# Kernel optimization log

Hardware: AMD Instinct MI355X
Metric: run time of the kernel (lower is better)

The kernel has to match this reference:

```python
import jax, jax.numpy as jnp
import numpy as np

# static config (matches init_kwargs / source constants)
B, S, CCH, NF, T = 64, 50, 3, 129, 29   # batch, seq, channels, freq bins (nfft/2+1), frames
M_FB = 32                                # filterbank size M in F1
D = 16                                   # latents -> SPD matrix size
M_OFF = D * (D - 1) // 2                 # strictly-lower Cholesky entries
HID = D + M_OFF                          # ODE state size
ODE_U = 256                              # n_units
NCLS = 5
K_EULER, DT = 4, 0.25                    # fixed-step Euler ODE solve per interval
BN_EPS = 1e-5


def lin_tri_filter(nfilt=M_FB, nfft=256, samplerate=100):
    # faithful port of FilterbankShape.lin_tri_filter_shape
    highfreq = samplerate / 2
    hz = np.linspace(0, highfreq, nfilt + 2)
    b = np.floor((nfft + 1) * hz / samplerate)
    fb = np.zeros([nfilt, nfft // 2 + 1])
    for j in range(nfilt):
        for i in range(int(b[j]), int(b[j + 1])):
            fb[j, i] = (i - b[j]) / (b[j + 1] - b[j])
        for i in range(int(b[j + 1]), int(b[j + 2])):
            fb[j, i] = (b[j + 2] - i) / (b[j + 2] - b[j + 1])
    return fb.T.astype(np.float32)  # (129, 32)


def setup_inputs() -> dict:
    key = jax.random.key(0)
    ks = jax.random.split(key, 32)
    f32 = jnp.float32
    CIN = CCH * M_FB  # 96

    def unif(k, shape, bound):
        return jax.random.uniform(k, shape, f32, -bound, bound)

    sd = 1.0 / np.sqrt(D)
    so = 1.0 / np.sqrt(M_OFF)
    cb1 = 1.0 / np.sqrt(CIN * 5)
    cb2 = 1.0 / np.sqrt(CIN * 5)
    lb = lambda fan_in: 1.0 / np.sqrt(fan_in)

    inp = {
        "x": jax.random.normal(ks[0], (B, S, CCH, NF, T), f32),
        "fw": jax.nn.sigmoid(jax.random.normal(ks[1], (NF, M_FB), f32)),
        "s_tri": jnp.asarray(lin_tri_filter()),
        "conv1_w": unif(ks[2], (CIN, CIN, 5), cb1),
        "conv1_b": unif(ks[3], (CIN,), cb1),
        "bn1_g": jnp.ones((CIN,), f32),
        "bn1_b": jnp.zeros((CIN,), f32),
        "conv2_w": unif(ks[4], (D, CIN, 5), cb2),
        "conv2_b": unif(ks[5], (D,), cb2),
        "bn2_g": jnp.ones((D,), f32),
        "bn2_b": jnp.zeros((D,), f32),
        "wx_d": unif(ks[6], (D, 3 * D), sd),
        "wh_d": unif(ks[7], (D, 3 * D), sd),
        "bias_d": unif(ks[8], (3 * D,), sd),
        "wx_o": unif(ks[9], (M_OFF, 3 * M_OFF), so),
        "wh_o": unif(ks[10], (M_OFF, 3 * M_OFF), so),
        "bias_o": unif(ks[11], (3 * M_OFF,), so),
        "ode_w0": unif(ks[12], (HID, ODE_U), lb(HID)),
        "ode_b0": unif(ks[13], (ODE_U,), lb(HID)),
        "ode_w1": unif(ks[14], (ODE_U, ODE_U), lb(ODE_U)),
        "ode_b1": unif(ks[15], (ODE_U,), lb(ODE_U)),
        "ode_w2": unif(ks[16], (ODE_U, ODE_U), lb(ODE_U)),
        "ode_b2": unif(ks[17], (ODE_U,), lb(ODE_U)),
        "ode_w3": unif(ks[18], (ODE_U, HID), lb(ODE_U)),
        "ode_b3": unif(ks[19], (HID,), lb(ODE_U)),
        "cls_w": unif(ks[20], (HID, NCLS), lb(HID)),
        "cls_b": unif(ks[21], (NCLS,), lb(HID)),
    }
    return inp


def _forward(x, fw, s_tri, conv1_w, conv1_b, bn1_g, bn1_b, conv2_w, conv2_b,
             bn2_g, bn2_b, wx_d, wh_d, bias_d, wx_o, wh_o, bias_o,
             ode_w0, ode_b0, ode_w1, ode_b1, ode_w2, ode_b2, ode_w3, ode_b3,
             cls_w, cls_b):
    b, s = x.shape[:2]
    # --- filter_bank: (b,s,C,F,T) x (F,M) -> (b,s,C*M,T) ---
    xf = jnp.einsum('bscft,fm->bscmt', x, fw * s_tri)
    h = xf.reshape(b * s, CCH * M_FB, T)
    dn = ('NCH', 'OIH', 'NCH')

    def conv_bn_lrelu(h, w, bias, g, be):
        h = jax.lax.conv_general_dilated(h, w, (1,), 'VALID', dimension_numbers=dn)
        h = h + bias[None, :, None]
        mu = h.mean((0, 2), keepdims=True)           # BatchNorm1d (train-mode stats)
        var = h.var((0, 2), keepdims=True)
        h = (h - mu) / jnp.sqrt(var + BN_EPS) * g[None, :, None] + be[None, :, None]
        return jnp.where(h >= 0, h, 0.01 * h)        # LeakyReLU

    h = conv_bn_lrelu(h, conv1_w, conv1_b, bn1_g, bn1_b)   # (bs, 96, 25)
    h = conv_bn_lrelu(h, conv2_w, conv2_b, bn2_g, bn2_b)   # (bs, D, 21)
    feats = h.transpose(0, 2, 1)                           # (bs, t, D)

    def oas(X):  # OAS-shrunk covariance, X: (n, d)
        n, d = X.shape
        xm = X - X.mean(0)
        emp = xm.T @ xm / (n - 1)
        mu = jnp.trace(emp) / d
        alpha = jnp.mean(emp ** 2)
        num = alpha + mu ** 2
        den = (n + 1.0) * (alpha - mu ** 2 / d)
        shr = jnp.where(den == 0, 1.0, jnp.minimum(num / den, 1.0))
        return (1.0 - shr) * emp + shr * mu * jnp.eye(d, dtype=X.dtype)

    covs = jax.vmap(oas)(feats)                            # (bs, D, D)
    L = jnp.linalg.cholesky(covs).reshape(b, s, D, D)
    ir, ic = np.tril_indices(D, -1)
    x_d = jnp.diagonal(L, axis1=-2, axis2=-1)              # (b,s,D) positive
    x_o = L[..., ir, ic]                                   # (b,s,M_OFF)

    def ode_net(hh):  # odefunc: Lin, [Tanh,Lin]*2, Tanh, Lin
        hh = hh @ ode_w0 + ode_b0
        hh = jnp.tanh(hh) @ ode_w1 + ode_b1
        hh = jnp.tanh(hh) @ ode_w2 + ode_b2
        return jnp.tanh(hh) @ ode_w3 + ode_b3

    abs_bd = jnp.abs(bias_d)

    def step(carry, xt):
        hd, ho = carry
        xd, xo = xt
        # ODE evolution of hidden state in Cholesky chart (log-diag || off-diag)
        hc = jnp.concatenate([jnp.log(hd), ho], -1)
        for _ in range(K_EULER):
            hc = hc + DT * ode_net(hc)
        hd = jnp.exp(hc[:, :D])
        ho = hc[:, D:]
        # diag RGRU cell (PosLinear + softplus; log/exp products simplify)
        gx = xd @ jnp.abs(wx_d)
        gh = hd @ jnp.abs(wh_d)
        ixr, ixi, ixn = jnp.split(gx, 3, 1)
        hhr, hhi, hhn = jnp.split(gh, 3, 1)
        br, bi, bn = jnp.split(abs_bd, 3)
        r = jax.nn.sigmoid(br * ixr * hhr)
        z = jax.nn.sigmoid(bi * ixi * hhi)
        ng = jax.nn.softplus(bn * ixn * r * hhn)
        hd = hd ** z * ng ** (1.0 - z)   # geodesic GRU update on positive diag
        # off-diag RGRU cell (standard Euclidean GRU)
        gx = xo @ wx_o
        gh = ho @ wh_o
        ixr, ixi, ixn = jnp.split(gx, 3, 1)
        hhr, hhi, hhn = jnp.split(gh, 3, 1)
        br2, bi2, bn2 = jnp.split(bias_o, 3)
        r = jax.nn.sigmoid(ixr + hhr + br2)
        z = jax.nn.sigmoid(ixi + hhi + bi2)
        ng = jnp.tanh(ixn + r * hhn + bn2)
        ho = ng + z * (ho - ng)
        return (hd, ho), None

    hd0 = jnp.ones((b, D), x.dtype)
    ho0 = jnp.zeros((b, M_OFF), x.dtype)
    (hd, ho), _ = jax.lax.scan(step, (hd0, ho0),
                               (x_d.transpose(1, 0, 2), x_o.transpose(1, 0, 2)))
    feat = jnp.concatenate([jnp.log(hd), ho], -1)
    return feat @ cls_w + cls_b  # (b, NCLS)


def reference(x, fw, s_tri, conv1_w, conv1_b, bn1_g, bn1_b, conv2_w, conv2_b,
              bn2_g, bn2_b, wx_d, wh_d, bias_d, wx_o, wh_o, bias_o,
              ode_w0, ode_b0, ode_w1, ode_b1, ode_w2, ode_b2, ode_w3, ode_b3,
              cls_w, cls_b):
    return _forward(x, fw, s_tri, conv1_w, conv1_b, bn1_g, bn1_b, conv2_w,
                    conv2_b, bn2_g, bn2_b, wx_d, wh_d, bias_d, wx_o, wh_o,
                    bias_o, ode_w0, ode_b0, ode_w1, ode_b1, ode_w2, ode_b2,
                    ode_w3, ode_b3, cls_w, cls_b)
```

## Files before the change

kernel.cpp:

```cpp
#include <hip/hip_runtime.h>
#include <math.h>


#define BB 64
#define NIMG 3200

typedef _Float16 f16;
typedef _Float16 f16x8 __attribute__((ext_vector_type(8)));
typedef float f32x4 __attribute__((ext_vector_type(4)));

#define HS 164
#define GS 516

__device__ __forceinline__ float sigm(float x) { return 1.f / (1.f + expf(-x)); }
__device__ __forceinline__ float fsigm(float x) {
  return __fdividef(1.f, 1.f + __expf(-x));
}
__device__ __forceinline__ float ftanh(float x) {
  return 1.f - __fdividef(2.f, __expf(2.f * x) + 1.f);
}

#define OFF_W0  0
#define OFF_W1  20480
#define OFF_W2  53248
#define OFF_W3  86016
#define OFF_GRZ 104448
#define OFF_GNX 135168
#define OFF_GNH 143360
#define PK2_TOT 151552

__global__ __launch_bounds__(256) void k1_fb(const float* __restrict__ x,
                                             const float* __restrict__ fw,
                                             const float* __restrict__ st,
                                             float* __restrict__ h1) {
  __shared__ __align__(16) float ws[129 * 32];
  __shared__ __align__(16) float xs[129 * 32];
  const int tid = threadIdx.x;
  const int n = blockIdx.x;
  const float* xp = x + (size_t)n * 11223;

  for (int i = tid; i < 4128; i += 256) ws[i] = fw[i] * st[i];

  float acc[4][4];
#pragma unroll
  for (int i = 0; i < 4; ++i)
#pragma unroll
    for (int j = 0; j < 4; ++j) acc[i][j] = 0.f;

  const int c = tid / 64;
  const int rem = tid % 64;
  const int m0 = (rem / 8) * 4;
  const int t0 = (rem % 8) * 4;

  for (int fc = 0; fc < 3; ++fc) {
    __syncthreads();
    for (int i = tid; i < 3741; i += 256) {
      int cc = i / 1247;
      int r = i - cc * 1247;
      int f = r / 29;
      int t = r - f * 29;
      xs[(cc * 43 + f) * 32 + t] = xp[cc * 3741 + (fc * 43 + f) * 29 + t];
    }
    for (int i = tid; i < 129; i += 256) {
      xs[i * 32 + 29] = 0.f; xs[i * 32 + 30] = 0.f; xs[i * 32 + 31] = 0.f;
    }
    __syncthreads();
    if (tid < 192) {
      const float* xb = xs + (c * 43) * 32 + t0;
      const float* wb = ws + (fc * 43) * 32 + m0;
      for (int f = 0; f < 43; ++f) {
        float4 xv = *(const float4*)(xb + f * 32);
        float4 wv = *(const float4*)(wb + f * 32);
        float xa[4] = {xv.x, xv.y, xv.z, xv.w};
        float wa[4] = {wv.x, wv.y, wv.z, wv.w};
#pragma unroll
        for (int i = 0; i < 4; ++i)
#pragma unroll
          for (int j = 0; j < 4; ++j) acc[i][j] += wa[i] * xa[j];
      }
    }
  }
  if (tid < 192) {
    const int nt = (t0 == 28) ? 1 : 4;
    for (int i = 0; i < 4; ++i)
      for (int j = 0; j < nt; ++j)
        h1[(size_t)n * 2784 + (size_t)(c * 32 + m0 + i) * 29 + (t0 + j)] = acc[i][j];
  }
}

__global__ __launch_bounds__(256) void k2_conv1(const float* __restrict__ h1,
                                                const float* __restrict__ w,
                                                const float* __restrict__ bias,
                                                float* __restrict__ h2,
                                                float* __restrict__ part1) {
  __shared__ __align__(16) float ins[2 * 96 * 32];
  __shared__ __align__(16) float wls[96 * 81];
  const int tid = threadIdx.x;
  const int wg = blockIdx.x;

  for (int i = tid; i < 2 * 2784; i += 256) {
    int img = i / 2784;
    int e = i - img * 2784;
    int ci = e / 29;
    int t = e - ci * 29;
    ins[img * 3072 + ci * 32 + t] = h1[(size_t)(wg * 2 + img) * 2784 + e];
  }

  const int img = tid / 96;
  const int co = tid - img * 96;
  float acc[25];
#pragma unroll
  for (int t = 0; t < 25; ++t) acc[t] = 0.f;

  for (int cc = 0; cc < 6; ++cc) {
    __syncthreads();
    for (int i = tid; i < 7680; i += 256) {
      int cw = i / 80;
      int r = i - cw * 80;
      wls[cw * 81 + r] = w[cw * 480 + cc * 80 + r];
    }
    __syncthreads();
    if (tid < 192) {
      for (int ci = 0; ci < 16; ++ci) {
        float xv[29];
#pragma unroll
        for (int j = 0; j < 29; ++j) xv[j] = ins[img * 3072 + (cc * 16 + ci) * 32 + j];
        float wv[5];
#pragma unroll
        for (int d = 0; d < 5; ++d) wv[d] = wls[co * 81 + ci * 5 + d];
#pragma unroll
        for (int t = 0; t < 25; ++t) {
          float s = acc[t];
#pragma unroll
          for (int d = 0; d < 5; ++d) s += xv[t + d] * wv[d];
          acc[t] = s;
        }
      }
    }
  }
  if (tid < 192) {
    const int n = wg * 2 + img;
    const float bval = bias[co];
    float s1 = 0.f, s2 = 0.f;
    for (int t = 0; t < 25; ++t) {
      float v = acc[t] + bval;
      h2[(size_t)n * 2400 + co * 25 + t] = v;
      s1 += v;
      s2 += v * v;
    }
    part1[((size_t)n * 96 + co) * 2 + 0] = s1;
    part1[((size_t)n * 96 + co) * 2 + 1] = s2;
  }
}

__global__ __launch_bounds__(256) void k3_bn1(const float* __restrict__ part,
                                              const float* __restrict__ gg,
                                              const float* __restrict__ be,
                                              float* __restrict__ ab) {
  __shared__ double sd[256], sq[256];
  const int c = blockIdx.x;
  const int t = threadIdx.x;
  double s = 0.0, q = 0.0;
  for (int n = t; n < NIMG; n += 256) {
    s += (double)part[((size_t)n * 96 + c) * 2 + 0];
    q += (double)part[((size_t)n * 96 + c) * 2 + 1];
  }
  sd[t] = s; sq[t] = q;
  __syncthreads();
  for (int off = 128; off > 0; off >>= 1) {
    if (t < off) { sd[t] += sd[t + off]; sq[t] += sq[t + off]; }
    __syncthreads();
  }
  if (t == 0) {
    double mu = sd[0] / 80000.0;
    double var = sq[0] / 80000.0 - mu * mu;
    float A = (float)((double)gg[c] / sqrt(var + 1e-5));
    ab[c * 2 + 0] = A;
    ab[c * 2 + 1] = (float)((double)be[c] - mu * (double)A);
  }
}

__global__ __launch_bounds__(256) void k5_bn2(const float* __restrict__ part,
                                              const float* __restrict__ gg,
                                              const float* __restrict__ be,
                                              float* __restrict__ ab) {
  __shared__ double sd[256], sq[256];
  const int c = blockIdx.x;
  const int t = threadIdx.x;
  double s = 0.0, q = 0.0;
  for (int n = t; n < 800; n += 256) {
    s += (double)part[((size_t)n * 16 + c) * 2 + 0];
    q += (double)part[((size_t)n * 16 + c) * 2 + 1];
  }
  sd[t] = s; sq[t] = q;
  __syncthreads();
  for (int off = 128; off > 0; off >>= 1) {
    if (t < off) { sd[t] += sd[t + off]; sq[t] += sq[t + off]; }
    __syncthreads();
  }
  if (t == 0) {
    double mu = sd[0] / 67200.0;
    double var = sq[0] / 67200.0 - mu * mu;
    float A = (float)((double)gg[c] / sqrt(var + 1e-5));
    ab[c * 2 + 0] = A;
    ab[c * 2 + 1] = (float)((double)be[c] - mu * (double)A);
  }
}

__global__ __launch_bounds__(256) void k4_conv2(const float* __restrict__ h2,
                                                const float* __restrict__ w,
                                                const float* __restrict__ bias,
                                                const float* __restrict__ bn1,
                                                float* __restrict__ h3,
                                                float* __restrict__ part2) {
  __shared__ __align__(16) float ins[4 * 96 * 26];
  __shared__ __align__(16) float wls[16 * 241];
  __shared__ float A1s[96], B1s[96];
  __shared__ float red[16 * 16 * 2];
  const int tid = threadIdx.x;
  const int wg = blockIdx.x;

  if (tid < 96) {
    A1s[tid] = bn1[tid * 2 + 0];
    B1s[tid] = bn1[tid * 2 + 1];
  }
  __syncthreads();
  for (int i = tid; i < 9600; i += 256) {
    int img = i / 2400;
    int e = i - img * 2400;
    int ci = e / 25;
    int t = e - ci * 25;
    float v = h2[(size_t)(wg * 4 + img) * 2400 + e];
    v = A1s[ci] * v + B1s[ci];
    v = (v >= 0.f) ? v : 0.01f * v;
    ins[img * 2496 + ci * 26 + t] = v;
  }
  for (int i = tid; i < 4 * 96; i += 256) ins[(i / 96) * 2496 + (i % 96) * 26 + 25] = 0.f;

  const int img = tid >> 6;
  const int co = (tid >> 2) & 15;
  const int tg = tid & 3;
  const int t0s[4] = {0, 6, 11, 16};
  const int t0 = t0s[tg];
  const int tl = (tg == 0) ? 6 : 5;
  float acc[6] = {0.f, 0.f, 0.f, 0.f, 0.f, 0.f};

  for (int cc = 0; cc < 2; ++cc) {
    __syncthreads();
    for (int i = tid; i < 3840; i += 256) {
      int cw = i / 240;
      int r = i - cw * 240;
      wls[cw * 241 + r] = w[cw * 480 + cc * 240 + r];
    }
    __syncthreads();
    for (int ci = 0; ci < 48; ++ci) {
      float xv[10];
#pragma unroll
      for (int j = 0; j < 10; ++j) xv[j] = ins[img * 2496 + (cc * 48 + ci) * 26 + t0 + j];
      float wv[5];
#pragma unroll
      for (int d = 0; d < 5; ++d) wv[d] = wls[co * 241 + ci * 5 + d];
#pragma unroll
      for (int t = 0; t < 6; ++t) {
        float s = acc[t];
#pragma unroll
        for (int d = 0; d < 5; ++d) s += xv[t + d] * wv[d];
        acc[t] = s;
      }
    }
  }
  const float bval = bias[co];
  float s1 = 0.f, s2 = 0.f;
  const int n = wg * 4 + img;
  for (int t = 0; t < 6; ++t) {
    if (t < tl) {
      float v = acc[t] + bval;
      h3[(size_t)n * 336 + co * 21 + t0 + t] = v;
      s1 += v;
      s2 += v * v;
    }
  }
  red[(co * 16 + img * 4 + tg) * 2 + 0] = s1;
  red[(co * 16 + img * 4 + tg) * 2 + 1] = s2;
  __syncthreads();
  if (tid < 16) {
    float s = 0.f, q = 0.f;
    for (int k = 0; k < 16; ++k) {
      s += red[(tid * 16 + k) * 2 + 0];
      q += red[(tid * 16 + k) * 2 + 1];
    }
    part2[((size_t)wg * 16 + tid) * 2 + 0] = s;
    part2[((size_t)wg * 16 + tid) * 2 + 1] = q;
  }
}

__global__ __launch_bounds__(256) void k6_oas(const float* __restrict__ h3,
                                              const float* __restrict__ bn2,
                                              float* __restrict__ xd,
                                              float* __restrict__ xo) {
  __shared__ float X[4][21 * 17 + 3];
  __shared__ float A[4][16 * 17];
  __shared__ float mcol[4][16];
  const int tid = threadIdx.x;
  const int wid = tid >> 6;
  const int lane = tid & 63;
  const int n = blockIdx.x * 4 + wid;
  const float* hp = h3 + (size_t)n * 336;

  for (int e = lane; e < 336; e += 64) {
    int c = e / 21;
    int t = e - c * 21;
    float v = hp[e];
    v = bn2[c * 2 + 0] * v + bn2[c * 2 + 1];
    v = (v >= 0.f) ? v : 0.01f * v;
    X[wid][t * 17 + c] = v;
  }
  __syncthreads();
  if (lane < 16) {
    float s = 0.f;
    for (int t = 0; t < 21; ++t) s += X[wid][t * 17 + lane];
    mcol[wid][lane] = s * (1.f / 21.f);
  }
  __syncthreads();
  for (int e = lane; e < 336; e += 64) {
    int t = e / 16;
    int c = e - t * 16;
    X[wid][t * 17 + c] -= mcol[wid][c];
  }
  __syncthreads();

  float tr_p = 0.f, al_p = 0.f;
  float ent[3];
  int ei[3], ej[3], ne = 0;
  for (int e = lane; e < 136; e += 64) {
    int i = 0, e2 = e;
    while (e2 >= 16 - i) { e2 -= 16 - i; i++; }
    int j = i + e2;
    float s = 0.f;
    for (int t = 0; t < 21; ++t) s += X[wid][t * 17 + i] * X[wid][t * 17 + j];
    s *= (1.f / 20.f);
    ent[ne] = s; ei[ne] = i; ej[ne] = j; ne++;
    if (i == j) tr_p += s;
    al_p += s * s * ((i == j) ? 1.f : 2.f);
  }
  for (int m = 1; m < 64; m <<= 1) {
    tr_p += __shfl_xor(tr_p, m);
    al_p += __shfl_xor(al_p, m);
  }
  const float mu = tr_p * (1.f / 16.f);
  const float alpha = al_p * (1.f / 256.f);
  const float num = alpha + mu * mu;
  const float den = 22.f * (alpha - mu * mu * (1.f / 16.f));
  const float shr = (den == 0.f) ? 1.f : fminf(num / den, 1.f);
  for (int q = 0; q < ne; ++q) {
    float c = (1.f - shr) * ent[q] + ((ei[q] == ej[q]) ? shr * mu : 0.f);
    A[wid][ei[q] * 17 + ej[q]] = c;
    A[wid][ej[q] * 17 + ei[q]] = c;
  }
  __syncthreads();

  for (int k = 0; k < 16; ++k) {
    float akk = A[wid][k * 17 + k];
    __syncthreads();
    float d = sqrtf(akk);
    float rd = 1.f / d;
    if (lane == k) A[wid][k * 17 + k] = d;
    if (lane > k && lane < 16) A[wid][lane * 17 + k] *= rd;
    __syncthreads();
    if (lane > k && lane < 16) {
      float Lik = A[wid][lane * 17 + k];
      for (int j = k + 1; j <= lane; ++j) A[wid][lane * 17 + j] -= Lik * A[wid][j * 17 + k];
    }
    __syncthreads();
  }
  if (lane < 16) xd[(size_t)n * 16 + lane] = A[wid][lane * 17 + lane];
  for (int p = lane; p < 120; p += 64) {
    int i = 1, p2 = p;
    while (p2 >= i) { p2 -= i; i++; }
    xo[(size_t)n * 120 + p] = A[wid][i * 17 + p2];
  }
}

__global__ __launch_bounds__(256) void k0_pack(const float* __restrict__ w0,
                                               const float* __restrict__ w1,
                                               const float* __restrict__ w2,
                                               const float* __restrict__ w3,
                                               const float* __restrict__ wxo,
                                               const float* __restrict__ who,
                                               uint32_t* __restrict__ dst) {
  int i = blockIdx.x * 256 + threadIdx.x;
  if (i >= PK2_TOT) return;
  int j = i, kind, NT;
  if (j < OFF_W1)       { kind = 0; NT = 16; }
  else if (j < OFF_W2)  { kind = 1; NT = 16; j -= OFF_W1; }
  else if (j < OFF_W3)  { kind = 2; NT = 16; j -= OFF_W2; }
  else if (j < OFF_GRZ) { kind = 3; NT = 9;  j -= OFF_W3; }
  else if (j < OFF_GNX) { kind = 4; NT = 15; j -= OFF_GRZ; }
  else if (j < OFF_GNH) { kind = 5; NT = 8;  j -= OFF_GNX; }
  else                  { kind = 6; NT = 8;  j -= OFF_GNH; }
  const int tile = j >> 8;
  const int rem = j & 255;
  const int l = rem >> 2;
  const int wd = rem & 3;
  const int t = tile / NT;
  const int nt = tile - t * NT;
  const int col = nt * 16 + (l & 15);
  const int kk = t * 32 + 8 * (l >> 4) + 2 * wd;

  float v[2];
#pragma unroll
  for (int q = 0; q < 2; ++q) {
    const int k = kk + q;
    float s = 0.f;
    if (kind == 0)      { if (k < 136) s = w0[k * 256 + col]; }
    else if (kind == 1) { s = w1[k * 256 + col]; }
    else if (kind == 2) { s = w2[k * 256 + col]; }
    else if (kind == 3) { if (col < 136) s = w3[k * 136 + col]; }
    else if (kind == 4) {
      if (k < 120) s = wxo[k * 360 + col];
      else if (k >= 128 && k < 248) s = who[(k - 128) * 360 + col];
    } else if (kind == 5) { if (k < 120 && col < 120) s = wxo[k * 360 + 240 + col]; }
    else                  { if (k < 120 && col < 120) s = who[k * 360 + 240 + col]; }
    v[q] = s;
  }
  union { f16 h[2]; uint32_t u; } cv;
  cv.h[0] = (f16)v[0];
  cv.h[1] = (f16)v[1];
  dst[i] = cv.u;
}

__device__ __forceinline__ uint4 aread_lin(const f16* X, int t, int l) {
  return ((const uint4*)X)[t * 64 + l];
}
__device__ __forceinline__ void xwrite_frag(f16* X, int row, int col, float v) {
  const int slot = row + 16 * ((col >> 3) & 3);
  const int byte = (((col >> 5) * 64 + slot) << 4) + 2 * (col & 7);
  *(f16*)((char*)X + byte) = (f16)v;
}

union UF { uint4 u; f16x8 h; };

template <int KT, int NT, int MODE>
__device__ __forceinline__ void mlp_one(const f16* __restrict__ Xin,
                                        const uint4* __restrict__ B,
                                        const float* __restrict__ bias,
                                        f16* __restrict__ Xout,
                                        float* __restrict__ hcf,
                                        f16* __restrict__ Xnext,
                                        float* __restrict__ ehl,
                                        int nt, int l) {
  if (nt < 0 || nt >= NT) return;
  const int m = l & 15;
  const int g = l >> 4;
  uint4 bf[KT];
#pragma unroll
  for (int t = 0; t < KT; ++t) bf[t] = B[(t * NT + nt) * 64 + l];
  uint4 af[KT];
#pragma unroll
  for (int t = 0; t < KT; ++t) af[t] = aread_lin(Xin, t, l);
  f32x4 acc = {0.f, 0.f, 0.f, 0.f};
#pragma unroll
  for (int t = 0; t < KT; ++t) {
    UF a; a.u = af[t];
    UF b; b.u = bf[t];
    acc = __builtin_amdgcn_mfma_f32_16x16x32_f16(a.h, b.h, acc, 0, 0, 0);
  }
  const int col = nt * 16 + m;
  if (MODE == 0) {
    const float bb = bias[col];
#pragma unroll
    for (int i2 = 0; i2 < 4; ++i2)
      xwrite_frag(Xout, 4 * g + i2, col, ftanh(acc[i2] + bb));
  } else {
    if (col < 136) {
      const float bb = bias[col];
#pragma unroll
      for (int i2 = 0; i2 < 4; ++i2) {
        const int row = 4 * g + i2;
        float v = hcf[row * HS + col] + 0.25f * (acc[i2] + bb);
        hcf[row * HS + col] = v;
        if (MODE == 1) {
          xwrite_frag(Xnext, row, col, v);
        } else {
          if (col >= 16) xwrite_frag(Xnext, row, col + 112, v);
          else ehl[row * 16 + col] = __expf(v);
        }
      }
    }
  }
}

template <int KT, int NT>
__device__ __forceinline__ void gate_tile(const f16* __restrict__ Xin,
                                          const uint4* __restrict__ B,
                                          float* __restrict__ GO,
                                          int nt, int ktoff, int gooff, int l) {
  if (nt < 0) return;
  const int m = l & 15;
  const int g = l >> 4;
  uint4 bf[KT];
#pragma unroll
  for (int t = 0; t < KT; ++t) bf[t] = B[(t * NT + nt) * 64 + l];
  uint4 af[KT];
#pragma unroll
  for (int t = 0; t < KT; ++t) af[t] = aread_lin(Xin, t + ktoff, l);
  f32x4 acc = {0.f, 0.f, 0.f, 0.f};
#pragma unroll
  for (int t = 0; t < KT; ++t) {
    UF a; a.u = af[t];
    UF b; b.u = bf[t];
    acc = __builtin_amdgcn_mfma_f32_16x16x32_f16(a.h, b.h, acc, 0, 0, 0);
  }
  const int col = nt * 16 + m;
#pragma unroll
  for (int i2 = 0; i2 < 4; ++i2)
    GO[(4 * g + i2) * GS + gooff + col] = acc[i2];
}

__global__ __launch_bounds__(1024, 1) void k7_scan(
    const float* __restrict__ xdv, const float* __restrict__ xov,
    const float* __restrict__ wxd, const float* __restrict__ whd,
    const float* __restrict__ bdv, const float* __restrict__ bov,
    const uint32_t* __restrict__ pk,
    const float* __restrict__ b0, const float* __restrict__ b1,
    const float* __restrict__ b2, const float* __restrict__ b3,
    const float* __restrict__ cw, const float* __restrict__ cbv,
    float* __restrict__ out) {
  __shared__ __align__(16) f16 XA[8 * 64 * 8];
  __shared__ __align__(16) f16 XB[8 * 64 * 8];
  __shared__ __align__(16) f16 XC[8 * 64 * 8];
  __shared__ __align__(16) f16 XG[8 * 64 * 8];
  __shared__ __align__(16) float GO[16 * GS];
  __shared__ __align__(16) float hcf[16 * HS];
  __shared__ __align__(16) float xdlv[16 * 16];
  __shared__ __align__(16) float ehl[16 * 16];
  __shared__ __align__(16) float G2[16 * 96];
  __shared__ __align__(16) float wdaT[48 * 16], whaT[48 * 16];
  __shared__ float b0l[256], b1l[256], b2l[256], b3l[144], bovl[360], bdvl[48];

  const int tid = threadIdx.x;
  const int w = tid >> 6;
  const int l = tid & 63;
  const int blk = blockIdx.x;

  const uint4* BW0 = (const uint4*)(pk + OFF_W0);
  const uint4* BW1 = (const uint4*)(pk + OFF_W1);
  const uint4* BW2 = (const uint4*)(pk + OFF_W2);
  const uint4* BW3 = (const uint4*)(pk + OFF_W3);
  const uint4* BRZ = (const uint4*)(pk + OFF_GRZ);
  const uint4* BNX = (const uint4*)(pk + OFF_GNX);
  const uint4* BNH = (const uint4*)(pk + OFF_GNH);

  for (int i = tid; i < 768; i += 1024) {
    int k = i / 48, c = i - k * 48;
    wdaT[c * 16 + k] = fabsf(wxd[i]);
    whaT[c * 16 + k] = fabsf(whd[i]);
  }
  for (int i = tid; i < 256; i += 1024) { b0l[i] = b0[i]; b1l[i] = b1[i]; b2l[i] = b2[i]; }
  if (tid < 144) b3l[tid] = (tid < 136) ? b3[tid] : 0.f;
  if (tid < 360) bovl[tid] = bov[tid];
  if (tid < 48) bdvl[tid] = fabsf(bdv[tid]);
  for (int i = tid; i < 16 * HS; i += 1024) hcf[i] = 0.f;
  for (int i = tid; i < 4096; i += 1024) { XA[i] = (f16)0.f; XG[i] = (f16)0.f; }
  __syncthreads();

#pragma unroll 1
  for (int s = 0; s < 50; ++s) {
#pragma unroll 1
    for (int e = 0; e < 4; ++e) {
      mlp_one<5, 16, 0>(XA, BW0, b0l, XB, nullptr, nullptr, nullptr, w, l);
      if (e == 0) {
        for (int i = tid; i < 1920; i += 1024) {
          int row = i / 120, c = i - row * 120;
          xwrite_frag(XG, row, c, xov[((size_t)(blk * 16 + row) * 50 + s) * 120 + c]);
        }
        if (tid < 256) {
          int row = tid >> 4, k = tid & 15;
          xdlv[tid] = xdv[((size_t)(blk * 16 + row) * 50 + s) * 16 + k];
        }
      }
      __syncthreads();
      mlp_one<8, 16, 0>(XB, BW1, b1l, XC, nullptr, nullptr, nullptr, w, l);
      __syncthreads();
      mlp_one<8, 16, 0>(XC, BW2, b2l, XB, nullptr, nullptr, nullptr, w, l);
      __syncthreads();
      if (e < 3)
        mlp_one<8, 9, 1>(XB, BW3, b3l, nullptr, hcf, XA, nullptr, w, l);
      else
        mlp_one<8, 9, 2>(XB, BW3, b3l, nullptr, hcf, XG, ehl, w, l);
      __syncthreads();
    }

    gate_tile<8, 15>(XG, BRZ, GO, (w < 15) ? w : -1, 0, 0, l);
    gate_tile<4, 8>(XG, BNX, GO, (w < 8) ? w : -1, 0, 256, l);
    gate_tile<4, 8>(XG, BNH, GO, (w >= 8) ? (w - 8) : -1, 4, 384, l);
    for (int i = tid; i < 1536; i += 1024) {
      int row = i / 96, c = i - row * 96;
      const float4* sv = (const float4*)((c < 48) ? &xdlv[row * 16] : &ehl[row * 16]);
      const float4* wv = (const float4*)((c < 48) ? &wdaT[c * 16] : &whaT[(c - 48) * 16]);
      float a = 0.f;
#pragma unroll
      for (int q = 0; q < 4; ++q) {
        float4 xq = sv[q], wq = wv[q];
        a += xq.x * wq.x + xq.y * wq.y + xq.z * wq.z + xq.w * wq.w;
      }
      G2[row * 96 + c] = a;
    }
    __syncthreads();

    for (int i = tid; i < 1920; i += 1024) {
      int row = i / 120, e2 = i - row * 120;
      float r = fsigm(GO[row * GS + e2] + bovl[e2]);
      float z = fsigm(GO[row * GS + 120 + e2] + bovl[120 + e2]);
      float ng = ftanh(GO[row * GS + 256 + e2] + r * GO[row * GS + 384 + e2] + bovl[240 + e2]);
      float ho = hcf[row * HS + 16 + e2];
      float v = ng + z * (ho - ng);
      hcf[row * HS + 16 + e2] = v;
      xwrite_frag(XA, row, 16 + e2, v);
    }
    if (tid < 256) {
      int row = tid >> 4, t = tid & 15;
      float ixr = G2[row * 96 + t], ixi = G2[row * 96 + 16 + t], ixn = G2[row * 96 + 32 + t];
      float hhr = G2[row * 96 + 48 + t], hhi = G2[row * 96 + 64 + t], hhn = G2[row * 96 + 80 + t];
      float br = bdvl[t], bi = bdvl[16 + t], bn = bdvl[32 + t];
      float r = fsigm(br * ixr * hhr);
      float z = fsigm(bi * ixi * hhi);
      float sp = bn * ixn * r * hhn;
      float ng = (sp > 20.f) ? sp : __logf(1.f + __expf(sp));
      float ldp = hcf[row * HS + t];
      float v = z * ldp + (1.f - z) * __logf(ng);
      hcf[row * HS + t] = v;
      xwrite_frag(XA, row, t, v);
    }
    __syncthreads();
  }

  if (tid < 80) {
    int row = tid / 5, c = tid - row * 5;
    float a = cbv[c];
    for (int k = 0; k < 136; ++k) a += hcf[row * HS + k] * cw[k * 5 + c];
    out[(size_t)(blk * 16 + row) * 5 + c] = a;
  }
}

extern "C" void kernel_launch(void* const* d_in, const int* in_sizes, int n_in,
                              void* d_out, int out_size, void* d_ws, size_t ws_size,
                              hipStream_t stream) {
  const float* x       = (const float*)d_in[0];
  const float* fw      = (const float*)d_in[1];
  const float* s_tri   = (const float*)d_in[2];
  const float* conv1_w = (const float*)d_in[3];
  const float* conv1_b = (const float*)d_in[4];
  const float* bn1_g   = (const float*)d_in[5];
  const float* bn1_b   = (const float*)d_in[6];
  const float* conv2_w = (const float*)d_in[7];
  const float* conv2_b = (const float*)d_in[8];
  const float* bn2_g   = (const float*)d_in[9];
  const float* bn2_b   = (const float*)d_in[10];
  const float* wx_d    = (const float*)d_in[11];
  const float* wh_d    = (const float*)d_in[12];
  const float* bias_d  = (const float*)d_in[13];
  const float* wx_o    = (const float*)d_in[14];
  const float* wh_o    = (const float*)d_in[15];
  const float* bias_o  = (const float*)d_in[16];
  const float* ode_w0  = (const float*)d_in[17];
  const float* ode_b0  = (const float*)d_in[18];
  const float* ode_w1  = (const float*)d_in[19];
  const float* ode_b1  = (const float*)d_in[20];
  const float* ode_w2  = (const float*)d_in[21];
  const float* ode_b2  = (const float*)d_in[22];
  const float* ode_w3  = (const float*)d_in[23];
  const float* ode_b3  = (const float*)d_in[24];
  const float* cls_w   = (const float*)d_in[25];
  const float* cls_b   = (const float*)d_in[26];

  float* ws = (float*)d_ws;
  float* h1  = ws;
  float* h3  = ws;
  float* xd  = ws + 1075200;
  float* xo  = ws + 1126400;
  float* h2  = ws + 8908800;
  float* p1  = ws + 16588800;
  float* bn1 = ws + 17203200;
  float* p2  = ws + 17203392;
  float* bn2 = ws + 17228992;
  uint32_t* pk = (uint32_t*)(ws + 8908800);

  hipLaunchKernelGGL(k1_fb,   dim3(NIMG),   dim3(256), 0, stream, x, fw, s_tri, h1);
  hipLaunchKernelGGL(k2_conv1,dim3(NIMG/2), dim3(256), 0, stream, h1, conv1_w, conv1_b, h2, p1);
  hipLaunchKernelGGL(k3_bn1,  dim3(96),     dim3(256), 0, stream, p1, bn1_g, bn1_b, bn1);
  hipLaunchKernelGGL(k4_conv2,dim3(NIMG/4), dim3(256), 0, stream, h2, conv2_w, conv2_b, bn1, h3, p2);
  hipLaunchKernelGGL(k5_bn2,  dim3(16),     dim3(256), 0, stream, p2, bn2_g, bn2_b, bn2);
  hipLaunchKernelGGL(k6_oas,  dim3(NIMG/4), dim3(256), 0, stream, h3, bn2, xd, xo);
  hipLaunchKernelGGL(k0_pack, dim3((PK2_TOT + 255) / 256), dim3(256), 0, stream,
                     ode_w0, ode_w1, ode_w2, ode_w3, wx_o, wh_o, pk);
  hipLaunchKernelGGL(k7_scan, dim3(4),      dim3(1024), 0, stream,
                     xd, xo, wx_d, wh_d, bias_d, bias_o, pk,
                     ode_b0, ode_b1, ode_b2, ode_b3, cls_w, cls_b, (float*)d_out);
}
```

Before: 1.927 ms.

## Halve scan block to 512 threads with two output tiles per wave

Cuts the sequential scan kernel from 16 to 8 waves per block. Each wave now computes two 16-column MFMA tiles (nt and nt+8) and shares the A-fragment loads between them. This lowers barrier cost and duplicated LDS A reads in a latency-bound recurrence. The cost is more serial MFMA and epilogue work per wave, fewer waves to hide latency, and higher register pressure.

```diff
diff --git a/kernel.cpp b/kernel.cpp
--- a/kernel.cpp
+++ b/kernel.cpp
@@ -12,7 +12,6 @@
 #define HS 164
 #define GS 516
 
-__device__ __forceinline__ float sigm(float x) { return 1.f / (1.f + expf(-x)); }
 __device__ __forceinline__ float fsigm(float x) {
   return __fdividef(1.f, 1.f + __expf(-x));
 }
@@ -440,31 +439,14 @@
 
 union UF { uint4 u; f16x8 h; };
 
-template <int KT, int NT, int MODE>
-__device__ __forceinline__ void mlp_one(const f16* __restrict__ Xin,
-                                        const uint4* __restrict__ B,
-                                        const float* __restrict__ bias,
-                                        f16* __restrict__ Xout,
-                                        float* __restrict__ hcf,
-                                        f16* __restrict__ Xnext,
-                                        float* __restrict__ ehl,
-                                        int nt, int l) {
-  if (nt < 0 || nt >= NT) return;
-  const int m = l & 15;
-  const int g = l >> 4;
-  uint4 bf[KT];
-#pragma unroll
-  for (int t = 0; t < KT; ++t) bf[t] = B[(t * NT + nt) * 64 + l];
-  uint4 af[KT];
-#pragma unroll
-  for (int t = 0; t < KT; ++t) af[t] = aread_lin(Xin, t, l);
-  f32x4 acc = {0.f, 0.f, 0.f, 0.f};
-#pragma unroll
-  for (int t = 0; t < KT; ++t) {
-    UF a; a.u = af[t];
-    UF b; b.u = bf[t];
-    acc = __builtin_amdgcn_mfma_f32_16x16x32_f16(a.h, b.h, acc, 0, 0, 0);
-  }
+template <int MODE>
+__device__ __forceinline__ void epi_do(int nt, f32x4 acc,
+                                       const float* __restrict__ bias,
+                                       f16* __restrict__ Xout,
+                                       float* __restrict__ hcf,
+                                       f16* __restrict__ Xnext,
+                                       float* __restrict__ ehl,
+                                       int m, int g) {
   const int col = nt * 16 + m;
   if (MODE == 0) {
     const float bb = bias[col];
@@ -490,34 +472,93 @@
   }
 }
 
-template <int KT, int NT>
-__device__ __forceinline__ void gate_tile(const f16* __restrict__ Xin,
-                                          const uint4* __restrict__ B,
-                                          float* __restrict__ GO,
-                                          int nt, int ktoff, int gooff, int l) {
-  if (nt < 0) return;
+template <int KT, int NT, int MODE>
+__device__ __forceinline__ void mlp_two(const f16* __restrict__ Xin,
+                                        const uint4* __restrict__ B,
+                                        const float* __restrict__ bias,
+                                        f16* __restrict__ Xout,
+                                        float* __restrict__ hcf,
+                                        f16* __restrict__ Xnext,
+                                        float* __restrict__ ehl,
+                                        int w, int l) {
   const int m = l & 15;
   const int g = l >> 4;
-  uint4 bf[KT];
-#pragma unroll
-  for (int t = 0; t < KT; ++t) bf[t] = B[(t * NT + nt) * 64 + l];
+  const int nt0 = w;
+  const int nt1 = w + 8;
+  const bool has1 = (nt1 < NT);
+  uint4 bf0[KT], bf1[KT];
+#pragma unroll
+  for (int t = 0; t < KT; ++t) bf0[t] = B[(t * NT + nt0) * 64 + l];
+  if (has1) {
+#pragma unroll
+    for (int t = 0; t < KT; ++t) bf1[t] = B[(t * NT + nt1) * 64 + l];
+  }
   uint4 af[KT];
 #pragma unroll
-  for (int t = 0; t < KT; ++t) af[t] = aread_lin(Xin, t + ktoff, l);
-  f32x4 acc = {0.f, 0.f, 0.f, 0.f};
+  for (int t = 0; t < KT; ++t) af[t] = aread_lin(Xin, t, l);
+  f32x4 acc0 = {0.f, 0.f, 0.f, 0.f};
+  f32x4 acc1 = {0.f, 0.f, 0.f, 0.f};
 #pragma unroll
   for (int t = 0; t < KT; ++t) {
     UF a; a.u = af[t];
-    UF b; b.u = bf[t];
-    acc = __builtin_amdgcn_mfma_f32_16x16x32_f16(a.h, b.h, acc, 0, 0, 0);
-  }
-  const int col = nt * 16 + m;
-#pragma unroll
-  for (int i2 = 0; i2 < 4; ++i2)
-    GO[(4 * g + i2) * GS + gooff + col] = acc[i2];
-}
-
-__global__ __launch_bounds__(1024, 1) void k7_scan(
+    UF b; b.u = bf0[t];
+    acc0 = __builtin_amdgcn_mfma_f32_16x16x32_f16(a.h, b.h, acc0, 0, 0, 0);
+    if (has1) {
+      UF c; c.u = bf1[t];
+      acc1 = __builtin_amdgcn_mfma_f32_16x16x32_f16(a.h, c.h, acc1, 0, 0, 0);
+    }
+  }
+  epi_do<MODE>(nt0, acc0, bias, Xout, hcf, Xnext, ehl, m, g);
+  if (has1) epi_do<MODE>(nt1, acc1, bias, Xout, hcf, Xnext, ehl, m, g);
+}
+
+template <int KT, int NT>
+__device__ __forceinline__ void gate_two(const f16* __restrict__ Xin,
+                                         const uint4* __restrict__ B,
+                                         float* __restrict__ GO,
+                                         int w, int ktoff, int gooff, int l) {
+  const int m = l & 15;
+  const int g = l >> 4;
+  const int nt0 = w;
+  const int nt1 = w + 8;
+  const bool has1 = (nt1 < NT);
+  uint4 bf0[KT], bf1[KT];
+#pragma unroll
+  for (int t = 0; t < KT; ++t) bf0[t] = B[(t * NT + nt0) * 64 + l];
+  if (has1) {
+#pragma unroll
+    for (int t = 0; t < KT; ++t) bf1[t] = B[(t * NT + nt1) * 64 + l];
+  }
+  uint4 af[KT];
+#pragma unroll
+  for (int t = 0; t < KT; ++t) af[t] = aread_lin(Xin, t + ktoff, l);
+  f32x4 acc0 = {0.f, 0.f, 0.f, 0.f};
+  f32x4 acc1 = {0.f, 0.f, 0.f, 0.f};
+#pragma unroll
+  for (int t = 0; t < KT; ++t) {
+    UF a; a.u = af[t];
+    UF b; b.u = bf0[t];
+    acc0 = __builtin_amdgcn_mfma_f32_16x16x32_f16(a.h, b.h, acc0, 0, 0, 0);
+    if (has1) {
+      UF c; c.u = bf1[t];
+      acc1 = __builtin_amdgcn_mfma_f32_16x16x32_f16(a.h, c.h, acc1, 0, 0, 0);
+    }
+  }
+  {
+    const int col = nt0 * 16 + m;
+#pragma unroll
+    for (int i2 = 0; i2 < 4; ++i2)
+      GO[(4 * g + i2) * GS + gooff + col] = acc0[i2];
+  }
+  if (has1) {
+    const int col = nt1 * 16 + m;
+#pragma unroll
+    for (int i2 = 0; i2 < 4; ++i2)
+      GO[(4 * g + i2) * GS + gooff + col] = acc1[i2];
+  }
+}
+
+__global__ __launch_bounds__(512, 1) void k7_scan(
     const float* __restrict__ xdv, const float* __restrict__ xov,
     const float* __restrict__ wxd, const float* __restrict__ whd,
     const float* __restrict__ bdv, const float* __restrict__ bov,
@@ -526,10 +567,10 @@
     const float* __restrict__ b2, const float* __restrict__ b3,
     const float* __restrict__ cw, const float* __restrict__ cbv,
     float* __restrict__ out) {
-  __shared__ __align__(16) f16 XA[8 * 64 * 8];
-  __shared__ __align__(16) f16 XB[8 * 64 * 8];
-  __shared__ __align__(16) f16 XC[8 * 64 * 8];
-  __shared__ __align__(16) f16 XG[8 * 64 * 8];
+  __shared__ __align__(16) f16 XA[16 * 256];
+  __shared__ __align__(16) f16 XB[16 * 256];
+  __shared__ __align__(16) f16 XC[16 * 256];
+  __shared__ __align__(16) f16 XG[16 * 256];
   __shared__ __align__(16) float GO[16 * GS];
   __shared__ __align__(16) float hcf[16 * HS];
   __shared__ __align__(16) float xdlv[16 * 16];
@@ -551,26 +592,26 @@
   const uint4* BNX = (const uint4*)(pk + OFF_GNX);
   const uint4* BNH = (const uint4*)(pk + OFF_GNH);
 
-  for (int i = tid; i < 768; i += 1024) {
+  for (int i = tid; i < 768; i += 512) {
     int k = i / 48, c = i - k * 48;
     wdaT[c * 16 + k] = fabsf(wxd[i]);
     whaT[c * 16 + k] = fabsf(whd[i]);
   }
-  for (int i = tid; i < 256; i += 1024) { b0l[i] = b0[i]; b1l[i] = b1[i]; b2l[i] = b2[i]; }
+  for (int i = tid; i < 256; i += 512) { b0l[i] = b0[i]; b1l[i] = b1[i]; b2l[i] = b2[i]; }
   if (tid < 144) b3l[tid] = (tid < 136) ? b3[tid] : 0.f;
   if (tid < 360) bovl[tid] = bov[tid];
   if (tid < 48) bdvl[tid] = fabsf(bdv[tid]);
-  for (int i = tid; i < 16 * HS; i += 1024) hcf[i] = 0.f;
-  for (int i = tid; i < 4096; i += 1024) { XA[i] = (f16)0.f; XG[i] = (f16)0.f; }
+  for (int i = tid; i < 16 * HS; i += 512) hcf[i] = 0.f;
+  for (int i = tid; i < 16 * 256; i += 512) { XA[i] = (f16)0.f; XG[i] = (f16)0.f; }
   __syncthreads();
 
 #pragma unroll 1
   for (int s = 0; s < 50; ++s) {
 #pragma unroll 1
     for (int e = 0; e < 4; ++e) {
-      mlp_one<5, 16, 0>(XA, BW0, b0l, XB, nullptr, nullptr, nullptr, w, l);
+      mlp_two<5, 16, 0>(XA, BW0, b0l, XB, nullptr, nullptr, nullptr, w, l);
       if (e == 0) {
-        for (int i = tid; i < 1920; i += 1024) {
+        for (int i = tid; i < 1920; i += 512) {
           int row = i / 120, c = i - row * 120;
           xwrite_frag(XG, row, c, xov[((size_t)(blk * 16 + row) * 50 + s) * 120 + c]);
         }
@@ -580,21 +621,21 @@
         }
       }
       __syncthreads();
-      mlp_one<8, 16, 0>(XB, BW1, b1l, XC, nullptr, nullptr, nullptr, w, l);
+      mlp_two<8, 16, 0>(XB, BW1, b1l, XC, nullptr, nullptr, nullptr, w, l);
       __syncthreads();
-      mlp_one<8, 16, 0>(XC, BW2, b2l, XB, nullptr, nullptr, nullptr, w, l);
+      mlp_two<8, 16, 0>(XC, BW2, b2l, XB, nullptr, nullptr, nullptr, w, l);
       __syncthreads();
       if (e < 3)
-        mlp_one<8, 9, 1>(XB, BW3, b3l, nullptr, hcf, XA, nullptr, w, l);
+        mlp_two<8, 9, 1>(XB, BW3, b3l, nullptr, hcf, XA, nullptr, w, l);
       else
-        mlp_one<8, 9, 2>(XB, BW3, b3l, nullptr, hcf, XG, ehl, w, l);
+        mlp_two<8, 9, 2>(XB, BW3, b3l, nullptr, hcf, XG, ehl, w, l);
       __syncthreads();
     }
 
-    gate_tile<8, 15>(XG, BRZ, GO, (w < 15) ? w : -1, 0, 0, l);
-    gate_tile<4, 8>(XG, BNX, GO, (w < 8) ? w : -1, 0, 256, l);
-    gate_tile<4, 8>(XG, BNH, GO, (w >= 8) ? (w - 8) : -1, 4, 384, l);
-    for (int i = tid; i < 1536; i += 1024) {
+    gate_two<8, 15>(XG, BRZ, GO, w, 0, 0, l);
+    gate_two<4, 8>(XG, BNX, GO, w, 0, 256, l);
+    gate_two<4, 8>(XG, BNH, GO, w, 4, 384, l);
+    for (int i = tid; i < 1536; i += 512) {
       int row = i / 96, c = i - row * 96;
       const float4* sv = (const float4*)((c < 48) ? &xdlv[row * 16] : &ehl[row * 16]);
       const float4* wv = (const float4*)((c < 48) ? &wdaT[c * 16] : &whaT[(c - 48) * 16]);
@@ -608,13 +649,13 @@
     }
     __syncthreads();
 
-    for (int i = tid; i < 1920; i += 1024) {
+    for (int i = tid; i < 1920; i += 512) {
       int row = i / 120, e2 = i - row * 120;
-      float r = fsigm(GO[row * GS + e2] + bovl[e2]);
-      float z = fsigm(GO[row * GS + 120 + e2] + bovl[120 + e2]);
-      float ng = ftanh(GO[row * GS + 256 + e2] + r * GO[row * GS + 384 + e2] + bovl[240 + e2]);
+      float rr = fsigm(GO[row * GS + e2] + bovl[e2]);
+      float zz = fsigm(GO[row * GS + 120 + e2] + bovl[120 + e2]);
+      float ng = ftanh(GO[row * GS + 256 + e2] + rr * GO[row * GS + 384 + e2] + bovl[240 + e2]);
       float ho = hcf[row * HS + 16 + e2];
-      float v = ng + z * (ho - ng);
+      float v = ng + zz * (ho - ng);
       hcf[row * HS + 16 + e2] = v;
       xwrite_frag(XA, row, 16 + e2, v);
     }
@@ -623,12 +664,12 @@
       float ixr = G2[row * 96 + t], ixi = G2[row * 96 + 16 + t], ixn = G2[row * 96 + 32 + t];
       float hhr = G2[row * 96 + 48 + t], hhi = G2[row * 96 + 64 + t], hhn = G2[row * 96 + 80 + t];
       float br = bdvl[t], bi = bdvl[16 + t], bn = bdvl[32 + t];
-      float r = fsigm(br * ixr * hhr);
-      float z = fsigm(bi * ixi * hhi);
-      float sp = bn * ixn * r * hhn;
+      float rr = fsigm(br * ixr * hhr);
+      float zz = fsigm(bi * ixi * hhi);
+      float sp = bn * ixn * rr * hhn;
       float ng = (sp > 20.f) ? sp : __logf(1.f + __expf(sp));
       float ldp = hcf[row * HS + t];
-      float v = z * ldp + (1.f - z) * __logf(ng);
+      float v = zz * ldp + (1.f - zz) * __logf(ng);
       hcf[row * HS + t] = v;
       xwrite_frag(XA, row, t, v);
     }
@@ -694,7 +735,7 @@
   hipLaunchKernelGGL(k6_oas,  dim3(NIMG/4), dim3(256), 0, stream, h3, bn2, xd, xo);
   hipLaunchKernelGGL(k0_pack, dim3((PK2_TOT + 255) / 256), dim3(256), 0, stream,
                      ode_w0, ode_w1, ode_w2, ode_w3, wx_o, wh_o, pk);
-  hipLaunchKernelGGL(k7_scan, dim3(4),      dim3(1024), 0, stream,
+  hipLaunchKernelGGL(k7_scan, dim3(4),      dim3(512), 0, stream,
                      xd, xo, wx_d, wh_d, bias_d, bias_o, pk,
                      ode_b0, ode_b1, ode_b2, ode_b3, cls_w, cls_b, (float*)d_out);
 }
```

Measured after the change: 2.096 ms. 1.09x slower.
